# Performance work log

Hardware: AMD Instinct MI355X
Metric: run time of the kernel (lower is better)

## Reference

```python
import jax, jax.numpy as jnp
import numpy as np

N_NODES = 100000
N_EDGES = 1600000
N_GRAPHS = 1024
F = 128
L = 3  # num_gnn_layers
EPS = 1e-5


def _ln(x, g, b):
    mu = jnp.mean(x, axis=-1, keepdims=True)
    v = jnp.mean((x - mu) ** 2, axis=-1, keepdims=True)
    return (x - mu) * jax.lax.rsqrt(v + EPS) * g + b


def setup_inputs() -> dict:
    key = jax.random.key(0)
    ks = jax.random.split(key, 40)
    s = 0.05
    d = {}
    d['x'] = jax.random.normal(ks[0], (N_NODES, F), jnp.float32)
    d['w'] = jax.random.uniform(ks[1], (N_NODES, 1), jnp.float32)
    d['edge_index'] = jax.random.randint(ks[2], (2, N_EDGES), 0, N_NODES)
    d['batch'] = jnp.sort(jax.random.randint(ks[3], (N_NODES,), 0, N_GRAPHS))
    # input linear: (monomer_features+1) -> gc_features
    d['W_in'] = jax.random.normal(ks[4], (F + 1, F), jnp.float32) * s
    d['b_in'] = jnp.zeros((F,), jnp.float32)
    # stacked GCBlock params [L, ...]
    d['sage_Wl'] = jax.random.normal(ks[5], (L, F, F), jnp.float32) * s
    d['sage_bl'] = jnp.zeros((L, F), jnp.float32)
    d['sage_Wr'] = jax.random.normal(ks[6], (L, F, F), jnp.float32) * s
    d['ln1_g'] = jnp.ones((L, F), jnp.float32)
    d['ln1_b'] = jnp.zeros((L, F), jnp.float32)
    d['lin1_W'] = jax.random.normal(ks[7], (L, F, F), jnp.float32) * s
    d['lin1_b'] = jnp.zeros((L, F), jnp.float32)
    d['lin2_W'] = jax.random.normal(ks[8], (L, F, F), jnp.float32) * s
    d['lin2_b'] = jnp.zeros((L, F), jnp.float32)
    d['ln2_g'] = jnp.ones((L, F), jnp.float32)
    d['ln2_b'] = jnp.zeros((L, F), jnp.float32)
    # MeanDiffFeatureBlock: Linear(2F -> F)
    d['mdf_W'] = jax.random.normal(ks[9], (2 * F, F), jnp.float32) * s
    d['mdf_b'] = jnp.zeros((F,), jnp.float32)
    # mean PoolingLayer params
    d['pln1_g'] = jnp.ones((F,), jnp.float32)
    d['pln1_b'] = jnp.zeros((F,), jnp.float32)
    d['plin1_W'] = jax.random.normal(ks[10], (F, F), jnp.float32) * s
    d['plin1_b'] = jnp.zeros((F,), jnp.float32)
    d['plin2_W'] = jax.random.normal(ks[11], (F, F), jnp.float32) * s
    d['plin2_b'] = jnp.zeros((F,), jnp.float32)
    d['pln2_g'] = jnp.ones((F,), jnp.float32)
    d['pln2_b'] = jnp.zeros((F,), jnp.float32)
    return d


def reference(x, w, edge_index, batch, W_in, b_in, sage_Wl, sage_bl, sage_Wr,
              ln1_g, ln1_b, lin1_W, lin1_b, lin2_W, lin2_b, ln2_g, ln2_b,
              mdf_W, mdf_b, pln1_g, pln1_b, plin1_W, plin1_b, plin2_W, plin2_b,
              pln2_g, pln2_b):
    src, dst = edge_index[0], edge_index[1]
    # in-degree for SAGE mean aggregation (clamped so isolated nodes -> 0 agg)
    deg = jax.ops.segment_sum(jnp.ones((N_EDGES,), jnp.float32), dst,
                              num_segments=N_NODES)
    deg = jnp.maximum(deg, 1.0)[:, None]
    # graph sizes for global_mean_pool
    cnt = jax.ops.segment_sum(jnp.ones((N_NODES,), jnp.float32), batch,
                              num_segments=N_GRAPHS)
    cnt = jnp.maximum(cnt, 1.0)[:, None]

    # inilinear on [x, weight-fraction]  (scalers are identity at init)
    h = jnp.concatenate([x, w], axis=-1) @ W_in + b_in  # [N, F]

    def gc_block(h, p):
        Wl, bl, Wr, g1, b1, W1, bb1, W2, bb2, g2, b2 = p
        # SAGEConv: lin_l(mean_j x_j) + lin_r(x_i)
        agg = jax.ops.segment_sum(h[src], dst, num_segments=N_NODES) / deg
        y = agg @ Wl + bl + h @ Wr
        y1 = _ln(y + h, g1, b1)
        y2 = jax.nn.elu(y1 @ W1 + bb1) @ W2 + bb2  # dropout = identity (eval)
        return _ln(y2 + y1, g2, b2), None

    h, _ = jax.lax.scan(gc_block, h,
                        (sage_Wl, sage_bl, sage_Wr, ln1_g, ln1_b,
                         lin1_W, lin1_b, lin2_W, lin2_b, ln2_g, ln2_b))

    # MeanDiffFeatureBlock
    gm = jax.ops.segment_sum(h, batch, num_segments=N_GRAPHS) / cnt  # [B, F]
    h = jnp.concatenate([h, h - gm[batch]], axis=-1) @ mdf_W + mdf_b

    # mean PoolingLayer
    p = jax.ops.segment_sum(h, batch, num_segments=N_GRAPHS) / cnt  # [B, F]
    hh = _ln(p, pln1_g, pln1_b)
    y = jax.nn.elu(hh @ plin1_W + plin1_b) @ plin2_W + plin2_b
    return _ln(y + hh, pln2_g, pln2_b)  # [B, F]
```

## Files before the change

kernel.cpp:

```cpp
#include <hip/hip_runtime.h>
#include <math.h>

#define NN 100000
#define NE 1600000
#define NG 1024
#define FF 128
#define BSH 9
#define NBK ((NN + 511) >> BSH)
#define RB 256
#define BCAP 16384

typedef __attribute__((ext_vector_type(8))) short short8;
typedef __attribute__((ext_vector_type(4))) float f32x4;
typedef __attribute__((ext_vector_type(2))) float f32x2;

__device__ __forceinline__ unsigned short f2b(float f) {
    union { float f; unsigned u; } v; v.f = f;
    unsigned r = (v.u + 0x7FFF + ((v.u >> 16) & 1)) >> 16;
    return (unsigned short)r;
}
__device__ __forceinline__ float us2f(unsigned short u) {
    union { unsigned u; float f; } v; v.u = ((unsigned)u) << 16; return v.f;
}
__device__ __forceinline__ float fast_elu(float v) {
    float e = __builtin_amdgcn_exp2f(v * 1.44269504088896340736f) - 1.0f;
    return v > 0.f ? v : e;
}
__device__ __forceinline__ uint2 pk8(const float* v) {
    unsigned lo = 0, hi = 0;
    lo = (unsigned)__builtin_amdgcn_cvt_pk_fp8_f32(v[0], v[1], (int)lo, false);
    lo = (unsigned)__builtin_amdgcn_cvt_pk_fp8_f32(v[2], v[3], (int)lo, true);
    hi = (unsigned)__builtin_amdgcn_cvt_pk_fp8_f32(v[4], v[5], (int)hi, false);
    hi = (unsigned)__builtin_amdgcn_cvt_pk_fp8_f32(v[6], v[7], (int)hi, true);
    uint2 r; r.x = lo; r.y = hi; return r;
}

__global__ void init_bcur(int* __restrict__ bcur) {
    int b = blockIdx.x * blockDim.x + threadIdx.x;
    if (b < NBK) bcur[b] = b * BCAP;
}

__global__ __launch_bounds__(256)
void radix_scatter(const int* __restrict__ src, const int* __restrict__ dst,
                   int* __restrict__ bcur, unsigned* __restrict__ pairs, int n) {
    __shared__ int base[NBK];
    __shared__ int cnt[NBK];
    for (int i = threadIdx.x; i < NBK; i += 256) cnt[i] = 0;
    __syncthreads();
    const int per = (n + RB - 1) / RB;
    const int beg = blockIdx.x * per;
    const int end = min(n, beg + per);
    for (int i = beg + threadIdx.x; i < end; i += 256)
        atomicAdd(&cnt[dst[i] >> BSH], 1);
    __syncthreads();
    for (int i = threadIdx.x; i < NBK; i += 256)
        base[i] = cnt[i] ? atomicAdd(&bcur[i], cnt[i]) : 0;
    __syncthreads();
    for (int i = beg + threadIdx.x; i < end; i += 256) {
        int d = dst[i];
        int p = atomicAdd(&base[d >> BSH], 1);
        pairs[p] = ((unsigned)src[i] << BSH) | (unsigned)(d & 511);
    }
}

__global__ __launch_bounds__(256)
void bucket_build(const unsigned* __restrict__ pairs, const int* __restrict__ bcur,
                  int* __restrict__ row_beg, int* __restrict__ row_end,
                  float* __restrict__ inv_deg, int* __restrict__ ssrc) {
    __shared__ int cnt[512];
    __shared__ int curs[512];
    __shared__ int wsum[4];
    const int b = blockIdx.x;
    const int n0 = b << BSH;
    const int t = threadIdx.x;
    const int lane = t & 63, wid = t >> 6;

    for (int i = t; i < 512; i += 256) cnt[i] = 0;
    __syncthreads();
    const int beg = b * BCAP, end = bcur[b];
    for (int i = beg + t; i < end; i += 256)
        atomicAdd(&cnt[pairs[i] & 511], 1);
    __syncthreads();

    int c0 = cnt[2 * t], c1 = cnt[2 * t + 1];
    int v = c0 + c1;
    int x = v;
    #pragma unroll
    for (int o = 1; o < 64; o <<= 1) {
        int y = __shfl_up(x, o);
        if (lane >= o) x += y;
    }
    if (lane == 63) wsum[wid] = x;
    __syncthreads();
    if (t == 0) {
        int s = 0;
        #pragma unroll
        for (int w2 = 0; w2 < 4; ++w2) { int tv = wsum[w2]; wsum[w2] = s; s += tv; }
    }
    __syncthreads();
    int g0 = beg + wsum[wid] + x - v;
    int g1 = g0 + c0;
    curs[2 * t] = g0;
    curs[2 * t + 1] = g1;
    {
        int node = n0 + 2 * t;
        if (node < NN) {
            row_beg[node] = g0; row_end[node] = g1;
            inv_deg[node] = 1.0f / (float)(c0 > 1 ? c0 : 1);
        }
        node = n0 + 2 * t + 1;
        if (node < NN) {
            row_beg[node] = g1; row_end[node] = g1 + c1;
            inv_deg[node] = 1.0f / (float)(c1 > 1 ? c1 : 1);
        }
    }
    __syncthreads();
    for (int i = beg + t; i < end; i += 256) {
        unsigned pr = pairs[i];
        int p = atomicAdd(&curs[pr & 511], 1);
        ssrc[p] = (int)(pr >> BSH) << 7;
    }
}

__global__ __launch_bounds__(256)
void graph_offsets(const int* __restrict__ batch, int* __restrict__ g_off,
                   float* __restrict__ inv_cnt) {
    int g = blockIdx.x * blockDim.x + threadIdx.x;
    if (g > NG) return;
    if (g == NG) { g_off[NG] = NN; return; }
    int lo = 0, hi = NN;
    while (lo < hi) { int mid = (lo + hi) >> 1; if (batch[mid] < g) lo = mid + 1; else hi = mid; }
    int lo2 = lo, hi2 = NN;
    while (lo2 < hi2) { int mid = (lo2 + hi2) >> 1; if (batch[mid] < g + 1) lo2 = mid + 1; else hi2 = mid; }
    g_off[g] = lo;
    int c = lo2 - lo;
    inv_cnt[g] = 1.0f / (float)(c > 1 ? c : 1);
}

struct WTab { const float* a[16]; };
__global__ __launch_bounds__(256)
void prep_weights(WTab tab, unsigned short* __restrict__ dst) {
    int w = blockIdx.x >> 6;
    int idx = ((blockIdx.x & 63) << 8) + threadIdx.x;
    int j = idx & 7, lane = (idx >> 3) & 63, nt = (idx >> 9) & 7, kc = idx >> 12;
    int cb = lane & 15, rq = lane >> 4;
    int k = kc * 32 + rq * 8 + j;
    int n = nt * 16 + cb;
    dst[(size_t)w * 16384 + idx] = f2b(tab.a[w][k * 128 + n]);
}

__global__ __launch_bounds__(256)
void sage_agg(const unsigned char* __restrict__ h8, const int* __restrict__ row_beg,
              const int* __restrict__ row_end, const float* __restrict__ inv_deg,
              const int* __restrict__ ssrc, unsigned short* __restrict__ aggb) {
    const int wid = threadIdx.x >> 6;
    const int lane = threadIdx.x & 63;
    const int node = blockIdx.x * 4 + wid;
    const int eg = lane >> 4, j = lane & 15;
    const int jo = j * 8;
    const int beg = row_beg[node], end = row_end[node];
    f32x2 a0 = {0.f, 0.f}, a1 = {0.f, 0.f}, a2 = {0.f, 0.f}, a3 = {0.f, 0.f};
    for (int e = beg + eg; e < end; e += 32) {
        uint2 u[8];
        #pragma unroll
        for (int k = 0; k < 8; ++k) {
            int ek = e + 4 * k;
            bool ok = ek < end;
            int idx = ssrc[ok ? ek : e];
            uint2 uu = *(const uint2*)(h8 + (unsigned)(idx + jo));
            uu.x = ok ? uu.x : 0u;
            uu.y = ok ? uu.y : 0u;
            u[k] = uu;
        }
        #pragma unroll
        for (int k = 0; k < 8; ++k) {
            a0 += __builtin_amdgcn_cvt_pk_f32_fp8(u[k].x, false);
            a1 += __builtin_amdgcn_cvt_pk_f32_fp8(u[k].x, true);
            a2 += __builtin_amdgcn_cvt_pk_f32_fp8(u[k].y, false);
            a3 += __builtin_amdgcn_cvt_pk_f32_fp8(u[k].y, true);
        }
    }
    float af[8] = {a0.x, a0.y, a1.x, a1.y, a2.x, a2.y, a3.x, a3.y};
    #pragma unroll
    for (int k = 0; k < 8; ++k) {
        af[k] += __shfl_xor(af[k], 16);
        af[k] += __shfl_xor(af[k], 32);
    }
    if (eg == 0) {
        float id = inv_deg[node];
        #pragma unroll
        for (int nt = 0; nt < 8; ++nt)
            aggb[(size_t)node * 128 + nt * 16 + j] = f2b(af[nt] * id);
    }
}

__global__ __launch_bounds__(128)
void pool_mean_b(const unsigned short* __restrict__ src, const int* __restrict__ g_off,
                 const float* __restrict__ inv_cnt, float* __restrict__ out) {
    const int g = blockIdx.x;
    const int j = threadIdx.x;
    const int beg = g_off[g], end = g_off[g + 1];
    float s = 0.f;
    for (int n = beg; n < end; ++n) s += us2f(src[(size_t)n * FF + j]);
    out[(size_t)g * FF + j] = s * inv_cnt[g];
}

template<bool AB16, bool R1, int RESM, int ACT, bool LN, bool OF32, bool OB16, bool OB8>
__global__ __launch_bounds__(256)
void gemm_mfma(const void* __restrict__ A_,
               const unsigned short* __restrict__ Wf,
               const float* __restrict__ bias,
               const float* __restrict__ rvec, const float* __restrict__ rrow,
               const float* __restrict__ res,
               const float* __restrict__ lng, const float* __restrict__ lnb,
               float* __restrict__ outf, unsigned short* __restrict__ outb,
               unsigned char* __restrict__ outb8, int M) {
    __shared__ short Al[64 * 136];

    const int t = threadIdx.x;
    const int lane = t & 63, wid = t >> 6;
    const int m0 = blockIdx.x * 64;
    const int cb = lane & 15, rq = lane >> 4;

    if (AB16) {
        const unsigned short* Ab = (const unsigned short*)A_;
        for (int i = t; i < 1024; i += 256) {
            int row = i >> 4, seg = i & 15;
            int gr = m0 + row; if (gr >= M) gr = M - 1;
            *(uint4*)&Al[row * 136 + seg * 8] = *(const uint4*)&Ab[(size_t)gr * 128 + seg * 8];
        }
    } else {
        const float* Af = (const float*)A_;
        for (int i = t; i < 2048; i += 256) {
            int row = i >> 5, seg = i & 31;
            int gr = m0 + row; if (gr >= M) gr = M - 1;
            float4 v = *(const float4*)&Af[(size_t)gr * 128 + seg * 4];
            ushort4 o = {f2b(v.x), f2b(v.y), f2b(v.z), f2b(v.w)};
            *(ushort4*)&Al[row * 136 + seg * 4] = o;
        }
    }
    __syncthreads();

    f32x4 acc[8];
    #pragma unroll
    for (int nt = 0; nt < 8; ++nt) acc[nt] = (f32x4){0.f, 0.f, 0.f, 0.f};

    const int aoff_base = (wid * 16 + cb) * 136 + rq * 8;
    for (int kc = 0; kc < 4; ++kc) {
        short8 a0 = *(const short8*)&Al[aoff_base + kc * 32];
        #pragma unroll
        for (int nt = 0; nt < 8; ++nt) {
            short8 b0 = *(const short8*)&Wf[(size_t)(kc * 8 + nt) * 512 + lane * 8];
            acc[nt] = __builtin_amdgcn_mfma_f32_16x16x32_bf16(a0, b0, acc[nt], 0, 0, 0);
        }
    }

    float bs[8], rr[8], lg[8], lb[8];
    #pragma unroll
    for (int nt = 0; nt < 8; ++nt) {
        int col = nt * 16 + cb;
        bs[nt] = bias[col];
        if (R1) rr[nt] = rrow[col];
        if (LN) { lg[nt] = lng[col]; lb[nt] = lnb[col]; }
    }
    #pragma unroll
    for (int reg = 0; reg < 4; ++reg) {
        int m = m0 + wid * 16 + rq * 4 + reg;
        int mc = m < M ? m : M - 1;
        float v[8];
        #pragma unroll
        for (int nt = 0; nt < 8; ++nt) v[nt] = acc[nt][reg] + bs[nt];
        if (R1) {
            float rv = rvec[mc];
            #pragma unroll
            for (int nt = 0; nt < 8; ++nt) v[nt] += rv * rr[nt];
        }
        if (RESM == 1) {
            #pragma unroll
            for (int nt = 0; nt < 8; ++nt) v[nt] += res[(size_t)mc * 128 + nt * 16 + cb];
        }
        if (ACT == 1) {
            #pragma unroll
            for (int nt = 0; nt < 8; ++nt) v[nt] = fast_elu(v[nt]);
        }
        if (LN) {
            float s1 = 0.f, s2 = 0.f;
            #pragma unroll
            for (int nt = 0; nt < 8; ++nt) { s1 += v[nt]; s2 += v[nt] * v[nt]; }
            #pragma unroll
            for (int o = 8; o >= 1; o >>= 1) { s1 += __shfl_xor(s1, o); s2 += __shfl_xor(s2, o); }
            float mu = s1 * (1.f / 128.f);
            float rs = rsqrtf(s2 * (1.f / 128.f) - mu * mu + 1e-5f);
            #pragma unroll
            for (int nt = 0; nt < 8; ++nt) v[nt] = (v[nt] - mu) * rs * lg[nt] + lb[nt];
        }
        if (m < M) {
            #pragma unroll
            for (int nt = 0; nt < 8; ++nt) {
                size_t o = (size_t)m * 128 + nt * 16 + cb;
                if (OF32) outf[o] = v[nt];
                if (OB16) outb[o] = f2b(v[nt]);
            }
            if (OB8) *(uint2*)&outb8[(size_t)m * 128 + cb * 8] = pk8(v);
        }
    }
}

__global__ __launch_bounds__(256)
void gc_chain(const unsigned short* __restrict__ hin, const unsigned short* __restrict__ aggb,
              unsigned short* __restrict__ hout, unsigned char* __restrict__ h8out,
              const unsigned short* __restrict__ Wl_f, const unsigned short* __restrict__ Wr_f,
              const unsigned short* __restrict__ W1_f, const unsigned short* __restrict__ W2_f,
              const float* __restrict__ bl,
              const float* __restrict__ g1, const float* __restrict__ b1,
              const float* __restrict__ bb1, const float* __restrict__ bb2,
              const float* __restrict__ g2, const float* __restrict__ b2, int M) {
    __shared__ short Hl[64 * 136];
    __shared__ short Gl[64 * 136];

    const int t = threadIdx.x;
    const int lane = t & 63, wid = t >> 6;
    const int m0 = blockIdx.x * 64;
    const int cb = lane & 15, rq = lane >> 4;
    const int aoff_base = (wid * 16 + cb) * 136 + rq * 8;
    const int boff = lane * 8;

    for (int i = t; i < 1024; i += 256) {
        int row = i >> 4, seg = i & 15;
        int gr = m0 + row; if (gr >= M) gr = M - 1;
        *(uint4*)&Hl[row * 136 + seg * 8] = *(const uint4*)&hin[(size_t)gr * 128 + seg * 8];
        *(uint4*)&Gl[row * 136 + seg * 8] = *(const uint4*)&aggb[(size_t)gr * 128 + seg * 8];
    }
    __syncthreads();

    f32x4 acc[8];
    #pragma unroll
    for (int nt = 0; nt < 8; ++nt) acc[nt] = (f32x4){0.f, 0.f, 0.f, 0.f};

    for (int kc = 0; kc < 4; ++kc) {
        short8 a0 = *(const short8*)&Gl[aoff_base + kc * 32];
        short8 a1 = *(const short8*)&Hl[aoff_base + kc * 32];
        #pragma unroll
        for (int nt = 0; nt < 8; ++nt) {
            const size_t wo = (size_t)(kc * 8 + nt) * 512 + boff;
            acc[nt] = __builtin_amdgcn_mfma_f32_16x16x32_bf16(a0, *(const short8*)&Wl_f[wo], acc[nt], 0, 0, 0);
            acc[nt] = __builtin_amdgcn_mfma_f32_16x16x32_bf16(a1, *(const short8*)&Wr_f[wo], acc[nt], 0, 0, 0);
        }
    }

    float y1r[4][8];
    {
        float bs[8], lg[8], lb[8];
        #pragma unroll
        for (int nt = 0; nt < 8; ++nt) {
            int col = nt * 16 + cb;
            bs[nt] = bl[col]; lg[nt] = g1[col]; lb[nt] = b1[col];
        }
        #pragma unroll
        for (int reg = 0; reg < 4; ++reg) {
            int r = wid * 16 + rq * 4 + reg;
            float v[8];
            float s1 = 0.f, s2 = 0.f;
            #pragma unroll
            for (int nt = 0; nt < 8; ++nt) {
                v[nt] = acc[nt][reg] + bs[nt] + us2f((unsigned short)Hl[r * 136 + nt * 16 + cb]);
                s1 += v[nt]; s2 += v[nt] * v[nt];
            }
            #pragma unroll
            for (int o = 8; o >= 1; o >>= 1) { s1 += __shfl_xor(s1, o); s2 += __shfl_xor(s2, o); }
            float mu = s1 * (1.f / 128.f);
            float rs = rsqrtf(s2 * (1.f / 128.f) - mu * mu + 1e-5f);
            #pragma unroll
            for (int nt = 0; nt < 8; ++nt) {
                float y = (v[nt] - mu) * rs * lg[nt] + lb[nt];
                y1r[reg][nt] = y;
                Hl[r * 136 + nt * 16 + cb] = (short)f2b(y);
            }
        }
    }

    #pragma unroll
    for (int nt = 0; nt < 8; ++nt) acc[nt] = (f32x4){0.f, 0.f, 0.f, 0.f};
    for (int kc = 0; kc < 4; ++kc) {
        short8 a0 = *(const short8*)&Hl[aoff_base + kc * 32];
        #pragma unroll
        for (int nt = 0; nt < 8; ++nt)
            acc[nt] = __builtin_amdgcn_mfma_f32_16x16x32_bf16(
                a0, *(const short8*)&W1_f[(size_t)(kc * 8 + nt) * 512 + boff], acc[nt], 0, 0, 0);
    }
    {
        float bs[8];
        #pragma unroll
        for (int nt = 0; nt < 8; ++nt) bs[nt] = bb1[nt * 16 + cb];
        #pragma unroll
        for (int reg = 0; reg < 4; ++reg) {
            int r = wid * 16 + rq * 4 + reg;
            #pragma unroll
            for (int nt = 0; nt < 8; ++nt) {
                float v = fast_elu(acc[nt][reg] + bs[nt]);
                Gl[r * 136 + nt * 16 + cb] = (short)f2b(v);
            }
        }
    }

    #pragma unroll
    for (int nt = 0; nt < 8; ++nt) acc[nt] = (f32x4){0.f, 0.f, 0.f, 0.f};
    for (int kc = 0; kc < 4; ++kc) {
        short8 a0 = *(const short8*)&Gl[aoff_base + kc * 32];
        #pragma unroll
        for (int nt = 0; nt < 8; ++nt)
            acc[nt] = __builtin_amdgcn_mfma_f32_16x16x32_bf16(
                a0, *(const short8*)&W2_f[(size_t)(kc * 8 + nt) * 512 + boff], acc[nt], 0, 0, 0);
    }
    {
        float bs[8], lg[8], lb[8];
        #pragma unroll
        for (int nt = 0; nt < 8; ++nt) {
            int col = nt * 16 + cb;
            bs[nt] = bb2[col]; lg[nt] = g2[col]; lb[nt] = b2[col];
        }
        #pragma unroll
        for (int reg = 0; reg < 4; ++reg) {
            int r = wid * 16 + rq * 4 + reg;
            int m = m0 + r;
            float v[8];
            float s1 = 0.f, s2 = 0.f;
            #pragma unroll
            for (int nt = 0; nt < 8; ++nt) {
                v[nt] = acc[nt][reg] + bs[nt] + y1r[reg][nt];
                s1 += v[nt]; s2 += v[nt] * v[nt];
            }
            #pragma unroll
            for (int o = 8; o >= 1; o >>= 1) { s1 += __shfl_xor(s1, o); s2 += __shfl_xor(s2, o); }
            float mu = s1 * (1.f / 128.f);
            float rs = rsqrtf(s2 * (1.f / 128.f) - mu * mu + 1e-5f);
            if (m < M) {
                float fv[8];
                #pragma unroll
                for (int nt = 0; nt < 8; ++nt) {
                    fv[nt] = (v[nt] - mu) * rs * lg[nt] + lb[nt];
                    hout[(size_t)m * 128 + nt * 16 + cb] = f2b(fv[nt]);
                }
                *(uint2*)&h8out[(size_t)m * 128 + cb * 8] = pk8(fv);
            }
        }
    }
}

extern "C" void kernel_launch(void* const* d_in, const int* in_sizes, int n_in,
                              void* d_out, int out_size, void* d_ws, size_t ws_size,
                              hipStream_t stream) {
    const float* x      = (const float*)d_in[0];
    const float* w      = (const float*)d_in[1];
    const int*   ei     = (const int*)d_in[2];
    const int*   batch  = (const int*)d_in[3];
    const float* W_in   = (const float*)d_in[4];
    const float* b_in   = (const float*)d_in[5];
    const float* sage_Wl = (const float*)d_in[6];
    const float* sage_bl = (const float*)d_in[7];
    const float* sage_Wr = (const float*)d_in[8];
    const float* ln1_g  = (const float*)d_in[9];
    const float* ln1_b  = (const float*)d_in[10];
    const float* lin1_W = (const float*)d_in[11];
    const float* lin1_b = (const float*)d_in[12];
    const float* lin2_W = (const float*)d_in[13];
    const float* lin2_b = (const float*)d_in[14];
    const float* ln2_g  = (const float*)d_in[15];
    const float* ln2_b  = (const float*)d_in[16];
    const float* mdf_W  = (const float*)d_in[17];
    const float* mdf_b  = (const float*)d_in[18];
    const float* pln1_g = (const float*)d_in[19];
    const float* pln1_b = (const float*)d_in[20];
    const float* plin1_W = (const float*)d_in[21];
    const float* plin1_b = (const float*)d_in[22];
    const float* plin2_W = (const float*)d_in[23];
    const float* plin2_b = (const float*)d_in[24];
    const float* pln2_g = (const float*)d_in[25];
    const float* pln2_b = (const float*)d_in[26];
    float* out = (float*)d_out;

    const int* e_src = ei;
    const int* e_dst = ei + NE;

    float* ws = (float*)d_ws;
    size_t off = 0;
    float* gm    = ws + off; off += (size_t)NG * FF;
    float* hh    = ws + off; off += (size_t)NG * FF;
    float* tt    = ws + off; off += (size_t)NG * FF;
    float* inv_deg = ws + off; off += NN;
    float* inv_cnt = ws + off; off += NG;
    unsigned short* us = (unsigned short*)(ws + off);
    size_t uoff = 0;
    unsigned short* hb0  = us + uoff; uoff += (size_t)NN * FF;
    unsigned short* hb1  = us + uoff; uoff += (size_t)NN * FF;
    unsigned short* aggb = us + uoff; uoff += (size_t)NN * FF;
    unsigned short* wt   = us + uoff; uoff += (size_t)16 * 16384;
    int* iw = (int*)(us + uoff);
    size_t ioff = 0;
    unsigned* pairs = (unsigned*)iw; ioff += (size_t)NBK * BCAP;
    int* ssrc    = iw + ioff; ioff += (size_t)NBK * BCAP;
    int* row_beg = iw + ioff; ioff += NN;
    int* row_end = iw + ioff; ioff += NN;
    int* g_off   = iw + ioff; ioff += NG + 1;
    int* bcur    = iw + ioff; ioff += NBK;
    unsigned char* h8 = (unsigned char*)pairs;

    WTab tab;
    tab.a[0] = W_in;
    for (int l = 0; l < 3; ++l) {
        tab.a[1 + l]  = sage_Wl + (size_t)l * 16384;
        tab.a[4 + l]  = sage_Wr + (size_t)l * 16384;
        tab.a[7 + l]  = lin1_W + (size_t)l * 16384;
        tab.a[10 + l] = lin2_W + (size_t)l * 16384;
    }
    tab.a[13] = mdf_W;
    tab.a[14] = plin1_W;
    tab.a[15] = plin2_W;
    prep_weights<<<16 * 64, 256, 0, stream>>>(tab, wt);
    const unsigned short* win_t = wt + 0 * 16384;
    const unsigned short* wa_t  = wt + 13 * 16384;
    const unsigned short* p1_t  = wt + 14 * 16384;
    const unsigned short* p2_t  = wt + 15 * 16384;

    init_bcur<<<1, 256, 0, stream>>>(bcur);
    graph_offsets<<<(NG + 256) / 256, 256, 0, stream>>>(batch, g_off, inv_cnt);
    radix_scatter<<<RB, 256, 0, stream>>>(e_src, e_dst, bcur, pairs, NE);
    bucket_build<<<NBK, 256, 0, stream>>>(pairs, bcur, row_beg, row_end, inv_deg, ssrc);

    const int GN = (NN + 63) / 64;
    const int GB = NG / 64;

    gemm_mfma<false, true, 0, 0, false, false, true, true><<<GN, 256, 0, stream>>>(
        x, win_t, b_in, w, W_in + 128 * 128,
        nullptr, nullptr, nullptr, nullptr, hb0, h8, NN);

    unsigned short* hcur = hb0;
    unsigned short* hnxt = hb1;
    for (int l = 0; l < 3; ++l) {
        sage_agg<<<NN / 4, 256, 0, stream>>>(h8, row_beg, row_end, inv_deg, ssrc, aggb);
        gc_chain<<<GN, 256, 0, stream>>>(
            hcur, aggb, hnxt, h8,
            wt + (size_t)(1 + l) * 16384, wt + (size_t)(4 + l) * 16384,
            wt + (size_t)(7 + l) * 16384, wt + (size_t)(10 + l) * 16384,
            sage_bl + (size_t)l * FF,
            ln1_g + (size_t)l * FF, ln1_b + (size_t)l * FF,
            lin1_b + (size_t)l * FF, lin2_b + (size_t)l * FF,
            ln2_g + (size_t)l * FF, ln2_b + (size_t)l * FF, NN);
        unsigned short* tmp = hcur; hcur = hnxt; hnxt = tmp;
    }

    pool_mean_b<<<NG, 128, 0, stream>>>(hcur, g_off, inv_cnt, gm);
    gemm_mfma<false, false, 0, 0, true, true, false, false><<<GB, 256, 0, stream>>>(
        gm, wa_t, mdf_b, nullptr, nullptr,
        nullptr, pln1_g, pln1_b, hh, nullptr, nullptr, NG);
    gemm_mfma<false, false, 0, 1, false, true, false, false><<<GB, 256, 0, stream>>>(
        hh, p1_t, plin1_b, nullptr, nullptr,
        nullptr, nullptr, nullptr, tt, nullptr, nullptr, NG);
    gemm_mfma<false, false, 1, 0, true, true, false, false><<<GB, 256, 0, stream>>>(
        tt, p2_t, plin2_b, nullptr, nullptr,
        hh, pln2_g, pln2_b, out, nullptr, nullptr, NG);
}
```

Before: 563.0 us.

## Widen sage_agg gathers to 16 bytes, vectorize pooling, fuse head GEMMs

The neighbor aggregation now has 8 lanes per edge, each loading 16 fp8 bytes, so there are fewer and wider gather loads; the output column mapping is adjusted to match. Graph mean pooling reads 8 bf16 values per lane across 4 row groups and reduces them with shuffles. The three small pooling-head GEMM kernels are fused into a single kernel that keeps intermediates in shared memory. The intent is to cut gather instruction count and launch overhead, at the cost of more accumulator registers and an extra shuffle stage.

After: 541.3 us. -3.8%, faster.

```diff
diff --git a/kernel.cpp b/kernel.cpp
--- a/kernel.cpp
+++ b/kernel.cpp
@@ -34,6 +34,7 @@
     hi = (unsigned)__builtin_amdgcn_cvt_pk_fp8_f32(v[6], v[7], (int)hi, true);
     uint2 r; r.x = lo; r.y = hi; return r;
 }
+#define MFMA(a, b, c) __builtin_amdgcn_mfma_f32_16x16x32_bf16((a), (b), (c), 0, 0, 0)
 
 __global__ void init_bcur(int* __restrict__ bcur) {
     int b = blockIdx.x * blockDim.x + threadIdx.x;
@@ -156,53 +157,79 @@
     const int wid = threadIdx.x >> 6;
     const int lane = threadIdx.x & 63;
     const int node = blockIdx.x * 4 + wid;
-    const int eg = lane >> 4, j = lane & 15;
-    const int jo = j * 8;
+    const int eg = lane >> 3, j8 = lane & 7;
+    const int jo = j8 * 16;
     const int beg = row_beg[node], end = row_end[node];
-    f32x2 a0 = {0.f, 0.f}, a1 = {0.f, 0.f}, a2 = {0.f, 0.f}, a3 = {0.f, 0.f};
+    f32x2 a[8];
+    #pragma unroll
+    for (int k = 0; k < 8; ++k) a[k] = (f32x2){0.f, 0.f};
     for (int e = beg + eg; e < end; e += 32) {
-        uint2 u[8];
-        #pragma unroll
-        for (int k = 0; k < 8; ++k) {
-            int ek = e + 4 * k;
+        uint4 u[4];
+        #pragma unroll
+        for (int k = 0; k < 4; ++k) {
+            int ek = e + 8 * k;
             bool ok = ek < end;
             int idx = ssrc[ok ? ek : e];
-            uint2 uu = *(const uint2*)(h8 + (unsigned)(idx + jo));
-            uu.x = ok ? uu.x : 0u;
-            uu.y = ok ? uu.y : 0u;
+            uint4 uu = *(const uint4*)(h8 + (unsigned)(idx + jo));
+            uu.x = ok ? uu.x : 0u; uu.y = ok ? uu.y : 0u;
+            uu.z = ok ? uu.z : 0u; uu.w = ok ? uu.w : 0u;
             u[k] = uu;
         }
         #pragma unroll
-        for (int k = 0; k < 8; ++k) {
-            a0 += __builtin_amdgcn_cvt_pk_f32_fp8(u[k].x, false);
-            a1 += __builtin_amdgcn_cvt_pk_f32_fp8(u[k].x, true);
-            a2 += __builtin_amdgcn_cvt_pk_f32_fp8(u[k].y, false);
-            a3 += __builtin_amdgcn_cvt_pk_f32_fp8(u[k].y, true);
-        }
-    }
-    float af[8] = {a0.x, a0.y, a1.x, a1.y, a2.x, a2.y, a3.x, a3.y};
-    #pragma unroll
-    for (int k = 0; k < 8; ++k) {
+        for (int k = 0; k < 4; ++k) {
+            a[0] += __builtin_amdgcn_cvt_pk_f32_fp8(u[k].x, false);
+            a[1] += __builtin_amdgcn_cvt_pk_f32_fp8(u[k].x, true);
+            a[2] += __builtin_amdgcn_cvt_pk_f32_fp8(u[k].y, false);
+            a[3] += __builtin_amdgcn_cvt_pk_f32_fp8(u[k].y, true);
+            a[4] += __builtin_amdgcn_cvt_pk_f32_fp8(u[k].z, false);
+            a[5] += __builtin_amdgcn_cvt_pk_f32_fp8(u[k].z, true);
+            a[6] += __builtin_amdgcn_cvt_pk_f32_fp8(u[k].w, false);
+            a[7] += __builtin_amdgcn_cvt_pk_f32_fp8(u[k].w, true);
+        }
+    }
+    float af[16];
+    #pragma unroll
+    for (int i = 0; i < 8; ++i) { af[2 * i] = a[i].x; af[2 * i + 1] = a[i].y; }
+    #pragma unroll
+    for (int k = 0; k < 16; ++k) {
+        af[k] += __shfl_xor(af[k], 8);
         af[k] += __shfl_xor(af[k], 16);
         af[k] += __shfl_xor(af[k], 32);
     }
     if (eg == 0) {
         float id = inv_deg[node];
         #pragma unroll
-        for (int nt = 0; nt < 8; ++nt)
-            aggb[(size_t)node * 128 + nt * 16 + j] = f2b(af[nt] * id);
-    }
-}
-
-__global__ __launch_bounds__(128)
+        for (int k = 0; k < 16; ++k) {
+            int p = jo + k;
+            int col = (p & 7) * 16 + (p >> 3);
+            aggb[(size_t)node * 128 + col] = f2b(af[k] * id);
+        }
+    }
+}
+
+__global__ __launch_bounds__(64)
 void pool_mean_b(const unsigned short* __restrict__ src, const int* __restrict__ g_off,
                  const float* __restrict__ inv_cnt, float* __restrict__ out) {
     const int g = blockIdx.x;
-    const int j = threadIdx.x;
+    const int lane = threadIdx.x & 63;
+    const int j = lane & 15, rs = lane >> 4;
     const int beg = g_off[g], end = g_off[g + 1];
-    float s = 0.f;
-    for (int n = beg; n < end; ++n) s += us2f(src[(size_t)n * FF + j]);
-    out[(size_t)g * FF + j] = s * inv_cnt[g];
+    float s[8] = {0.f, 0.f, 0.f, 0.f, 0.f, 0.f, 0.f, 0.f};
+    for (int n = beg + rs; n < end; n += 4) {
+        short8 v = *(const short8*)&src[(size_t)n * FF + j * 8];
+        #pragma unroll
+        for (int i = 0; i < 8; ++i) s[i] += us2f((unsigned short)v[i]);
+    }
+    #pragma unroll
+    for (int i = 0; i < 8; ++i) {
+        s[i] += __shfl_xor(s[i], 16);
+        s[i] += __shfl_xor(s[i], 32);
+    }
+    if (rs == 0) {
+        float ic = inv_cnt[g];
+        #pragma unroll
+        for (int i = 0; i < 8; ++i) out[(size_t)g * FF + j * 8 + i] = s[i] * ic;
+    }
 }
 
 template<bool AB16, bool R1, int RESM, int ACT, bool LN, bool OF32, bool OB16, bool OB8>
@@ -251,7 +278,7 @@
         #pragma unroll
         for (int nt = 0; nt < 8; ++nt) {
             short8 b0 = *(const short8*)&Wf[(size_t)(kc * 8 + nt) * 512 + lane * 8];
-            acc[nt] = __builtin_amdgcn_mfma_f32_16x16x32_bf16(a0, b0, acc[nt], 0, 0, 0);
+            acc[nt] = MFMA(a0, b0, acc[nt]);
         }
     }
 
@@ -343,8 +370,8 @@
         #pragma unroll
         for (int nt = 0; nt < 8; ++nt) {
             const size_t wo = (size_t)(kc * 8 + nt) * 512 + boff;
-            acc[nt] = __builtin_amdgcn_mfma_f32_16x16x32_bf16(a0, *(const short8*)&Wl_f[wo], acc[nt], 0, 0, 0);
-            acc[nt] = __builtin_amdgcn_mfma_f32_16x16x32_bf16(a1, *(const short8*)&Wr_f[wo], acc[nt], 0, 0, 0);
+            acc[nt] = MFMA(a0, *(const short8*)&Wl_f[wo], acc[nt]);
+            acc[nt] = MFMA(a1, *(const short8*)&Wr_f[wo], acc[nt]);
         }
     }
 
@@ -385,8 +412,7 @@
         short8 a0 = *(const short8*)&Hl[aoff_base + kc * 32];
         #pragma unroll
         for (int nt = 0; nt < 8; ++nt)
-            acc[nt] = __builtin_amdgcn_mfma_f32_16x16x32_bf16(
-                a0, *(const short8*)&W1_f[(size_t)(kc * 8 + nt) * 512 + boff], acc[nt], 0, 0, 0);
+            acc[nt] = MFMA(a0, *(const short8*)&W1_f[(size_t)(kc * 8 + nt) * 512 + boff], acc[nt]);
     }
     {
         float bs[8];
@@ -409,8 +435,7 @@
         short8 a0 = *(const short8*)&Gl[aoff_base + kc * 32];
         #pragma unroll
         for (int nt = 0; nt < 8; ++nt)
-            acc[nt] = __builtin_amdgcn_mfma_f32_16x16x32_bf16(
-                a0, *(const short8*)&W2_f[(size_t)(kc * 8 + nt) * 512 + boff], acc[nt], 0, 0, 0);
+            acc[nt] = MFMA(a0, *(const short8*)&W2_f[(size_t)(kc * 8 + nt) * 512 + boff], acc[nt]);
     }
     {
         float bs[8], lg[8], lb[8];
@@ -443,6 +468,133 @@
                 }
                 *(uint2*)&h8out[(size_t)m * 128 + cb * 8] = pk8(fv);
             }
+        }
+    }
+}
+
+__global__ __launch_bounds__(256)
+void head_chain(const float* __restrict__ gm,
+                const unsigned short* __restrict__ Wa_f,
+                const unsigned short* __restrict__ P1_f,
+                const unsigned short* __restrict__ P2_f,
+                const float* __restrict__ mdfb,
+                const float* __restrict__ g1, const float* __restrict__ b1,
+                const float* __restrict__ p1b, const float* __restrict__ p2b,
+                const float* __restrict__ g2, const float* __restrict__ b2,
+                float* __restrict__ outp) {
+    __shared__ short Al[64 * 136];
+
+    const int t = threadIdx.x;
+    const int lane = t & 63, wid = t >> 6;
+    const int m0 = blockIdx.x * 64;
+    const int cb = lane & 15, rq = lane >> 4;
+    const int aoff_base = (wid * 16 + cb) * 136 + rq * 8;
+    const int boff = lane * 8;
+
+    for (int i = t; i < 2048; i += 256) {
+        int row = i >> 5, seg = i & 31;
+        float4 v = *(const float4*)&gm[(size_t)(m0 + row) * 128 + seg * 4];
+        ushort4 o = {f2b(v.x), f2b(v.y), f2b(v.z), f2b(v.w)};
+        *(ushort4*)&Al[row * 136 + seg * 4] = o;
+    }
+    __syncthreads();
+
+    f32x4 acc[8];
+    #pragma unroll
+    for (int nt = 0; nt < 8; ++nt) acc[nt] = (f32x4){0.f, 0.f, 0.f, 0.f};
+    for (int kc = 0; kc < 4; ++kc) {
+        short8 a0 = *(const short8*)&Al[aoff_base + kc * 32];
+        #pragma unroll
+        for (int nt = 0; nt < 8; ++nt)
+            acc[nt] = MFMA(a0, *(const short8*)&Wa_f[(size_t)(kc * 8 + nt) * 512 + boff], acc[nt]);
+    }
+    float y1r[4][8];
+    {
+        float bs[8], lg[8], lb[8];
+        #pragma unroll
+        for (int nt = 0; nt < 8; ++nt) {
+            int col = nt * 16 + cb;
+            bs[nt] = mdfb[col]; lg[nt] = g1[col]; lb[nt] = b1[col];
+        }
+        #pragma unroll
+        for (int reg = 0; reg < 4; ++reg) {
+            int r = wid * 16 + rq * 4 + reg;
+            float v[8];
+            float s1 = 0.f, s2 = 0.f;
+            #pragma unroll
+            for (int nt = 0; nt < 8; ++nt) {
+                v[nt] = acc[nt][reg] + bs[nt];
+                s1 += v[nt]; s2 += v[nt] * v[nt];
+            }
+            #pragma unroll
+            for (int o = 8; o >= 1; o >>= 1) { s1 += __shfl_xor(s1, o); s2 += __shfl_xor(s2, o); }
+            float mu = s1 * (1.f / 128.f);
+            float rs = rsqrtf(s2 * (1.f / 128.f) - mu * mu + 1e-5f);
+            #pragma unroll
+            for (int nt = 0; nt < 8; ++nt) {
+                float y = (v[nt] - mu) * rs * lg[nt] + lb[nt];
+                y1r[reg][nt] = y;
+                Al[r * 136 + nt * 16 + cb] = (short)f2b(y);
+            }
+        }
+    }
+
+    #pragma unroll
+    for (int nt = 0; nt < 8; ++nt) acc[nt] = (f32x4){0.f, 0.f, 0.f, 0.f};
+    for (int kc = 0; kc < 4; ++kc) {
+        short8 a0 = *(const short8*)&Al[aoff_base + kc * 32];
+        #pragma unroll
+        for (int nt = 0; nt < 8; ++nt)
+            acc[nt] = MFMA(a0, *(const short8*)&P1_f[(size_t)(kc * 8 + nt) * 512 + boff], acc[nt]);
+    }
+    {
+        float bs[8];
+        #pragma unroll
+        for (int nt = 0; nt < 8; ++nt) bs[nt] = p1b[nt * 16 + cb];
+        #pragma unroll
+        for (int reg = 0; reg < 4; ++reg) {
+            int r = wid * 16 + rq * 4 + reg;
+            #pragma unroll
+            for (int nt = 0; nt < 8; ++nt) {
+                float v = fast_elu(acc[nt][reg] + bs[nt]);
+                Al[r * 136 + nt * 16 + cb] = (short)f2b(v);
+            }
+        }
+    }
+
+    #pragma unroll
+    for (int nt = 0; nt < 8; ++nt) acc[nt] = (f32x4){0.f, 0.f, 0.f, 0.f};
+    for (int kc = 0; kc < 4; ++kc) {
+        short8 a0 = *(const short8*)&Al[aoff_base + kc * 32];
+        #pragma unroll
+        for (int nt = 0; nt < 8; ++nt)
+            acc[nt] = MFMA(a0, *(const short8*)&P2_f[(size_t)(kc * 8 + nt) * 512 + boff], acc[nt]);
+    }
+    {
+        float bs[8], lg[8], lb[8];
+        #pragma unroll
+        for (int nt = 0; nt < 8; ++nt) {
+            int col = nt * 16 + cb;
+            bs[nt] = p2b[col]; lg[nt] = g2[col]; lb[nt] = b2[col];
+        }
+        #pragma unroll
+        for (int reg = 0; reg < 4; ++reg) {
+            int r = wid * 16 + rq * 4 + reg;
+            int m = m0 + r;
+            float v[8];
+            float s1 = 0.f, s2 = 0.f;
+            #pragma unroll
+            for (int nt = 0; nt < 8; ++nt) {
+                v[nt] = acc[nt][reg] + bs[nt] + y1r[reg][nt];
+                s1 += v[nt]; s2 += v[nt] * v[nt];
+            }
+            #pragma unroll
+            for (int o = 8; o >= 1; o >>= 1) { s1 += __shfl_xor(s1, o); s2 += __shfl_xor(s2, o); }
+            float mu = s1 * (1.f / 128.f);
+            float rs = rsqrtf(s2 * (1.f / 128.f) - mu * mu + 1e-5f);
+            #pragma unroll
+            for (int nt = 0; nt < 8; ++nt)
+                outp[(size_t)m * 128 + nt * 16 + cb] = (v[nt] - mu) * rs * lg[nt] + lb[nt];
         }
     }
 }
@@ -549,14 +701,9 @@
         unsigned short* tmp = hcur; hcur = hnxt; hnxt = tmp;
     }
 
-    pool_mean_b<<<NG, 128, 0, stream>>>(hcur, g_off, inv_cnt, gm);
-    gemm_mfma<false, false, 0, 0, true, true, false, false><<<GB, 256, 0, stream>>>(
-        gm, wa_t, mdf_b, nullptr, nullptr,
-        nullptr, pln1_g, pln1_b, hh, nullptr, nullptr, NG);
-    gemm_mfma<false, false, 0, 1, false, true, false, false><<<GB, 256, 0, stream>>>(
-        hh, p1_t, plin1_b, nullptr, nullptr,
-        nullptr, nullptr, nullptr, tt, nullptr, nullptr, NG);
-    gemm_mfma<false, false, 1, 0, true, true, false, false><<<GB, 256, 0, stream>>>(
-        tt, p2_t, plin2_b, nullptr, nullptr,
-        hh, pln2_g, pln2_b, out, nullptr, nullptr, NG);
-}
+    pool_mean_b<<<NG, 64, 0, stream>>>(hcur, g_off, inv_cnt, gm);
+    head_chain<<<GB, 256, 0, stream>>>(
+        gm, wa_t, p1_t, p2_t, mdf_b,
+        pln1_g, pln1_b, plin1_b, plin2_b, pln2_g, pln2_b, out);
+    (void)hh; (void)tt;
+}
```
